# Kernel tuning notes

Measured on AMD Instinct MI355X. Metric: run time of the kernel, lower is better.

## Reference

```python
import jax, jax.numpy as jnp
import numpy as np

B, P, G = 64, 512, 64      # batch of independent nets, populations, generator inputs
N = P + G                   # presynaptic channels per population
H = 32                      # neuron-MLP hidden width
DT = 0.1                    # integration step (ms)
EREV_MIN, EREV_MAX = -75.0, 0.0


def setup_inputs() -> dict:
    key = jax.random.key(0)
    ks = jax.random.split(key, 16)
    state = jax.random.uniform(ks[0], (B, P), dtype=jnp.float32)          # prev firing rates
    inp = jax.random.uniform(ks[1], (B, G), dtype=jnp.float32)            # generator rates
    R = jnp.ones((B, P, N), dtype=jnp.float32)                            # recovered resources
    U = jnp.zeros((B, P, N), dtype=jnp.float32)                           # utilization
    A = jnp.zeros((B, P, N), dtype=jnp.float32)                           # active resources
    gsyn_max = 2.0 * jax.random.uniform(ks[2], (P, N), dtype=jnp.float32)
    pconn = jax.random.uniform(ks[3], (P, N), dtype=jnp.float32)
    Uinc = 0.1 + 0.5 * jax.random.uniform(ks[4], (P, N), dtype=jnp.float32)
    tau_r = 100.0 + 400.0 * jax.random.uniform(ks[5], (P, N), dtype=jnp.float32)  # recovery (ms)
    tau_f = 10.0 + 50.0 * jax.random.uniform(ks[6], (P, N), dtype=jnp.float32)    # facilitation
    tau_d = 2.0 + 5.0 * jax.random.uniform(ks[7], (P, N), dtype=jnp.float32)      # decay
    Erev = jnp.where(jax.random.uniform(ks[8], (P, N)) > 0.5, 0.0, -75.0).astype(jnp.float32)
    mask = jnp.ones((P, N), dtype=bool)                                   # is_connected_mask
    Cm = 0.5 + 2.0 * jax.random.uniform(ks[9], (P,), dtype=jnp.float32)
    W1 = 0.5 * jax.random.normal(ks[10], (P, 2, H), dtype=jnp.float32)
    b1 = 0.5 * jax.random.normal(ks[11], (P, H), dtype=jnp.float32)
    W2 = 0.5 * jax.random.normal(ks[12], (P, H, 1), dtype=jnp.float32)
    b2 = 0.5 * jax.random.normal(ks[13], (P, 1), dtype=jnp.float32)
    return {"state": state, "inp": inp, "R": R, "U": U, "A": A,
            "gsyn_max": gsyn_max, "pconn": pconn, "Uinc": Uinc,
            "tau_r": tau_r, "tau_f": tau_f, "tau_d": tau_d,
            "Erev": Erev, "mask": mask, "Cm": Cm,
            "W1": W1, "b1": b1, "W2": W2, "b2": b2}


def reference(state, inp, R, U, A, gsyn_max, pconn, Uinc, tau_r, tau_f, tau_d,
              Erev, mask, Cm, W1, b1, W2, b2):
    # --- TimeStepLayer.call: concat prev state with generator input -> full presyn vector
    x = jnp.concatenate([state, inp], axis=-1)                  # [B, N]
    SR = x[:, None, :] * pconn                                  # [B, P, N] spike prob per conn

    # --- TsodycsMarkramSynapse one Euler step (all populations fused)
    e_d = jnp.exp(-DT / tau_d)
    e_r = jnp.exp(-DT / tau_r)
    e_f = jnp.exp(-DT / tau_f)
    tau1r = jnp.where(tau_d != tau_r, tau_d / (tau_d - tau_r), 1e-13)
    a_dec = A * e_d
    r_dec = 1.0 + (R - 1.0 + tau1r * U) * e_r - tau1r * U
    u_dec = U * e_f
    u0 = u_dec + Uinc * (1.0 - u_dec) * SR                      # new utilization
    a0 = a_dec + u0 * r_dec * SR                                # new active fraction

    # --- synaptic drive features per population
    g = gsyn_max * a0 * mask                                    # [B, P, N]
    g_tot = jnp.sum(g, axis=-1)                                 # [B, P]
    E_eff = jnp.sum(g * Erev, axis=-1) / (g_tot + 1e-8)
    E_norm = (E_eff - EREV_MIN) / (EREV_MAX - EREV_MIN)
    g_norm = g_tot / (g_tot + Cm[None, :])
    feat = jnp.stack([E_norm, g_norm], axis=-1)                 # [B, P, 2]

    # --- frozen per-population neuron net (square activation, sigmoid rate)
    h = jnp.square(jnp.einsum('bpf,pfh->bph', feat, W1) + b1)   # [B, P, H]
    out = jax.nn.sigmoid(jnp.einsum('bph,pho->bpo', h, W2) + b2)[..., 0]  # [B, P]
    return out
```

## Files before the change

kernel.cpp:

```cpp
#include <hip/hip_runtime.h>

#define PP 512
#define GG 64
#define NN 576

#define STEP(PC, UP, EF, ER, C1, ED, GS, GEp, Rv, Uv, Av, Xv, GT, GE)        \
  {                                                                          \
    float sr   = (Xv) * (PC);                                                \
    float udec = (Uv) * (EF);                                                \
    float u0   = udec + (UP) * (Xv) * (1.0f - udec);                         \
    float rdec = 1.0f + ((Rv) - 1.0f) * (ER) + (C1) * (Uv);                  \
    float a0   = (Av) * (ED) + u0 * rdec * sr;                               \
    GT = fmaf((GS), a0, GT);                                                 \
    GE = fmaf((GEp), a0, GE);                                                \
  }

__global__ __launch_bounds__(256, 4)
void timestep_kernel(const float* __restrict__ state,
                     const float* __restrict__ inp,
                     const float* __restrict__ R,
                     const float* __restrict__ U,
                     const float* __restrict__ A,
                     const float* __restrict__ gsyn_max,
                     const float* __restrict__ pconn,
                     const float* __restrict__ Uinc,
                     const float* __restrict__ tau_r,
                     const float* __restrict__ tau_f,
                     const float* __restrict__ tau_d,
                     const float* __restrict__ Erev,
                     const float* __restrict__ Cm,
                     const float* __restrict__ W1,
                     const float* __restrict__ b1,
                     const float* __restrict__ W2,
                     const float* __restrict__ b2,
                     float* __restrict__ out)
{
    __shared__ __align__(16) float Ppc[NN];
    __shared__ __align__(16) float Pup[NN];
    __shared__ __align__(16) float Pef[NN];
    __shared__ __align__(16) float Per[NN];
    __shared__ __align__(16) float Pc1[NN];
    __shared__ __align__(16) float Ped[NN];
    __shared__ __align__(16) float Pgs[NN];
    __shared__ __align__(16) float PgE[NN];

    const int tid  = threadIdx.x;
    const int lane = tid & 63;
    const int wave = tid >> 6;
    const int p    = blockIdx.x >> 1;
    const int half = blockIdx.x & 1;
    const int prow = p * NN;

    #pragma unroll
    for (int k = 0; k < 3; ++k) {
        int n = tid + k * 256;
        if (k < 2 || tid < 64) {
            const int o = prow + n;
            float tr = tau_r[o], tf = tau_f[o], td = tau_d[o];
            float pcv = pconn[o], ui = Uinc[o], gsv = gsyn_max[o], erv = Erev[o];
            float e_r = __expf(-0.1f * __builtin_amdgcn_rcpf(tr));
            float e_f = __expf(-0.1f * __builtin_amdgcn_rcpf(tf));
            float e_d = __expf(-0.1f * __builtin_amdgcn_rcpf(td));
            float diff = td - tr;
            float t1r  = (diff != 0.0f) ? td * __builtin_amdgcn_rcpf(diff) : 1e-13f;
            Ppc[n] = pcv;
            Pup[n] = ui * pcv;
            Pef[n] = e_f;
            Per[n] = e_r;
            Pc1[n] = t1r * (e_r - 1.0f);
            Ped[n] = e_d;
            Pgs[n] = gsv;
            PgE[n] = gsv * erv;
        }
    }

    const int   j   = lane & 31;
    const float w1a = W1[p * 64 + j];
    const float w1b = W1[p * 64 + 32 + j];
    const float b1j = b1[p * 32 + j];
    const float w2j = W2[p * 32 + j];
    const float b2p = b2[p];
    const float cmp = Cm[p];

    __syncthreads();

    const int bbase = half * 32 + wave * 8;
    #pragma unroll 1
    for (int pass = 0; pass < 4; ++pass) {
        const int b0  = bbase + pass * 2;
        const int b1i = b0 + 1;
        const size_t r0 = ((size_t)b0  * PP + p) * (size_t)NN;
        const size_t r1 = ((size_t)b1i * PP + p) * (size_t)NN;
        float gt0 = 0.0f, ge0 = 0.0f, gt1 = 0.0f, ge1 = 0.0f;

        #pragma unroll
        for (int c = 0; c < 2; ++c) {
            const int off = c * 64 + lane;
            const int np  = c * 256 + 4 * lane;
            float4 Ra = ((const float4*)R)[(r0 >> 2) + off];
            float4 Rb = ((const float4*)R)[(r1 >> 2) + off];
            float4 Ua = ((const float4*)U)[(r0 >> 2) + off];
            float4 Ub = ((const float4*)U)[(r1 >> 2) + off];
            float4 Aa = ((const float4*)A)[(r0 >> 2) + off];
            float4 Ab = ((const float4*)A)[(r1 >> 2) + off];
            float4 Xa = ((const float4*)state)[((b0  * PP) >> 2) + off];
            float4 Xb = ((const float4*)state)[((b1i * PP) >> 2) + off];
            float4 vpc = *(const float4*)&Ppc[np];
            float4 vup = *(const float4*)&Pup[np];
            float4 vef = *(const float4*)&Pef[np];
            float4 ver = *(const float4*)&Per[np];
            float4 vc1 = *(const float4*)&Pc1[np];
            float4 ved = *(const float4*)&Ped[np];
            float4 vgs = *(const float4*)&Pgs[np];
            float4 vgE = *(const float4*)&PgE[np];
            STEP(vpc.x, vup.x, vef.x, ver.x, vc1.x, ved.x, vgs.x, vgE.x,
                 Ra.x, Ua.x, Aa.x, Xa.x, gt0, ge0)
            STEP(vpc.y, vup.y, vef.y, ver.y, vc1.y, ved.y, vgs.y, vgE.y,
                 Ra.y, Ua.y, Aa.y, Xa.y, gt0, ge0)
            STEP(vpc.z, vup.z, vef.z, ver.z, vc1.z, ved.z, vgs.z, vgE.z,
                 Ra.z, Ua.z, Aa.z, Xa.z, gt0, ge0)
            STEP(vpc.w, vup.w, vef.w, ver.w, vc1.w, ved.w, vgs.w, vgE.w,
                 Ra.w, Ua.w, Aa.w, Xa.w, gt0, ge0)
            STEP(vpc.x, vup.x, vef.x, ver.x, vc1.x, ved.x, vgs.x, vgE.x,
                 Rb.x, Ub.x, Ab.x, Xb.x, gt1, ge1)
            STEP(vpc.y, vup.y, vef.y, ver.y, vc1.y, ved.y, vgs.y, vgE.y,
                 Rb.y, Ub.y, Ab.y, Xb.y, gt1, ge1)
            STEP(vpc.z, vup.z, vef.z, ver.z, vc1.z, ved.z, vgs.z, vgE.z,
                 Rb.z, Ub.z, Ab.z, Xb.z, gt1, ge1)
            STEP(vpc.w, vup.w, vef.w, ver.w, vc1.w, ved.w, vgs.w, vgE.w,
                 Rb.w, Ub.w, Ab.w, Xb.w, gt1, ge1)
        }
        {
            const int    nt = 512 + lane;
            const size_t oa = r0 + (size_t)nt;
            const size_t ob = r1 + (size_t)nt;
            float Rs0 = R[oa], Us0 = U[oa], As0 = A[oa];
            float Rs1 = R[ob], Us1 = U[ob], As1 = A[ob];
            float Xs0 = inp[b0  * GG + lane];
            float Xs1 = inp[b1i * GG + lane];
            float spc = Ppc[nt], sup = Pup[nt], sef = Pef[nt], ser = Per[nt];
            float sc1 = Pc1[nt], sed = Ped[nt], sgs = Pgs[nt], sgE = PgE[nt];
            STEP(spc, sup, sef, ser, sc1, sed, sgs, sgE,
                 Rs0, Us0, As0, Xs0, gt0, ge0)
            STEP(spc, sup, sef, ser, sc1, sed, sgs, sgE,
                 Rs1, Us1, As1, Xs1, gt1, ge1)
        }

        #pragma unroll
        for (int m = 32; m >= 1; m >>= 1) {
            gt0 += __shfl_xor(gt0, m, 64);
            gt1 += __shfl_xor(gt1, m, 64);
            ge0 += __shfl_xor(ge0, m, 64);
            ge1 += __shfl_xor(ge1, m, 64);
        }

        float En0 = (ge0 * __builtin_amdgcn_rcpf(gt0 + 1e-8f) + 75.0f) * (1.0f / 75.0f);
        float En1 = (ge1 * __builtin_amdgcn_rcpf(gt1 + 1e-8f) + 75.0f) * (1.0f / 75.0f);
        float gn0 = gt0 * __builtin_amdgcn_rcpf(gt0 + cmp);
        float gn1 = gt1 * __builtin_amdgcn_rcpf(gt1 + cmp);
        float pre0 = fmaf(En0, w1a, fmaf(gn0, w1b, b1j));
        float pre1 = fmaf(En1, w1a, fmaf(gn1, w1b, b1j));
        float v0 = pre0 * pre0 * w2j;
        float v1 = pre1 * pre1 * w2j;
        #pragma unroll
        for (int m = 16; m >= 1; m >>= 1) {
            v0 += __shfl_xor(v0, m, 64);
            v1 += __shfl_xor(v1, m, 64);
        }
        float s0 = v0 + b2p;
        float s1 = v1 + b2p;
        float o0 = __builtin_amdgcn_rcpf(1.0f + __expf(-s0));
        float o1 = __builtin_amdgcn_rcpf(1.0f + __expf(-s1));
        if (lane == 0) {
            out[(size_t)b0  * PP + p] = o0;
            out[(size_t)b1i * PP + p] = o1;
        }
    }
}

extern "C" void kernel_launch(void* const* d_in, const int* in_sizes, int n_in,
                              void* d_out, int out_size, void* d_ws, size_t ws_size,
                              hipStream_t stream) {
    const float* state = (const float*)d_in[0];
    const float* inp   = (const float*)d_in[1];
    const float* R     = (const float*)d_in[2];
    const float* U     = (const float*)d_in[3];
    const float* A     = (const float*)d_in[4];
    const float* gsyn  = (const float*)d_in[5];
    const float* pconn = (const float*)d_in[6];
    const float* Uinc  = (const float*)d_in[7];
    const float* taur  = (const float*)d_in[8];
    const float* tauf  = (const float*)d_in[9];
    const float* taud  = (const float*)d_in[10];
    const float* Erev  = (const float*)d_in[11];
    const float* Cm    = (const float*)d_in[13];
    const float* W1    = (const float*)d_in[14];
    const float* b1    = (const float*)d_in[15];
    const float* W2    = (const float*)d_in[16];
    const float* b2    = (const float*)d_in[17];
    float* out = (float*)d_out;

    hipLaunchKernelGGL(timestep_kernel, dim3(1024), dim3(256), 0, stream,
                       state, inp, R, U, A, gsyn, pconn, Uinc, taur, tauf, taud,
                       Erev, Cm, W1, b1, W2, b2, out);
}
```

Measured before the change: 282.5 us.

## Split batch across four blocks per population and fully unroll four batches per wave

Each population is now handled by four blocks of 16 batches instead of two blocks of 32, doubling the grid to 2048 blocks. Each wave processes four batch rows in one straight-line body, with all loads issued up front, replacing the rolled loop of two-row passes. The intent is more parallelism and more memory loads in flight to saturate HBM bandwidth on the streaming R/U/A reads. The cost is that the per-population parameter precompute (exp and reciprocal) is done twice as often, plus more register pressure now that the occupancy hint is gone from launch bounds.

```diff
diff --git a/kernel.cpp b/kernel.cpp
--- a/kernel.cpp
+++ b/kernel.cpp
@@ -15,7 +15,70 @@
     GE = fmaf((GEp), a0, GE);                                                \
   }
 
-__global__ __launch_bounds__(256, 4)
+#define PASSBODY(bb, GT, GE)                                                 \
+  {                                                                          \
+    const int b_  = (bb);                                                    \
+    const int r4_ = (b_ * PP + p) * (NN / 4);                                \
+    const int s4_ = (b_ * PP) >> 2;                                          \
+    float4 Ra = ((const float4*)R)[r4_ + lane];                              \
+    float4 Ua = ((const float4*)U)[r4_ + lane];                              \
+    float4 Aa = ((const float4*)A)[r4_ + lane];                              \
+    float4 Xa = ((const float4*)state)[s4_ + lane];                          \
+    float4 Rb = ((const float4*)R)[r4_ + 64 + lane];                         \
+    float4 Ub = ((const float4*)U)[r4_ + 64 + lane];                         \
+    float4 Ab = ((const float4*)A)[r4_ + 64 + lane];                         \
+    float4 Xb = ((const float4*)state)[s4_ + 64 + lane];                     \
+    const int ot_ = r4_ * 4 + 512 + lane;                                    \
+    float Rs = R[ot_];                                                       \
+    float Us = U[ot_];                                                       \
+    float As = A[ot_];                                                       \
+    float Xs = inp[b_ * GG + lane];                                          \
+    {                                                                        \
+      const int np = 4 * lane;                                               \
+      float4 vpc = *(const float4*)&Ppc[np];                                 \
+      float4 vup = *(const float4*)&Pup[np];                                 \
+      float4 vef = *(const float4*)&Pef[np];                                 \
+      float4 ver = *(const float4*)&Per[np];                                 \
+      float4 vc1 = *(const float4*)&Pc1[np];                                 \
+      float4 ved = *(const float4*)&Ped[np];                                 \
+      float4 vgs = *(const float4*)&Pgs[np];                                 \
+      float4 vgE = *(const float4*)&PgE[np];                                 \
+      STEP(vpc.x, vup.x, vef.x, ver.x, vc1.x, ved.x, vgs.x, vgE.x,           \
+           Ra.x, Ua.x, Aa.x, Xa.x, GT, GE)                                   \
+      STEP(vpc.y, vup.y, vef.y, ver.y, vc1.y, ved.y, vgs.y, vgE.y,           \
+           Ra.y, Ua.y, Aa.y, Xa.y, GT, GE)                                   \
+      STEP(vpc.z, vup.z, vef.z, ver.z, vc1.z, ved.z, vgs.z, vgE.z,           \
+           Ra.z, Ua.z, Aa.z, Xa.z, GT, GE)                                   \
+      STEP(vpc.w, vup.w, vef.w, ver.w, vc1.w, ved.w, vgs.w, vgE.w,           \
+           Ra.w, Ua.w, Aa.w, Xa.w, GT, GE)                                   \
+    }                                                                        \
+    {                                                                        \
+      const int np = 256 + 4 * lane;                                         \
+      float4 vpc = *(const float4*)&Ppc[np];                                 \
+      float4 vup = *(const float4*)&Pup[np];                                 \
+      float4 vef = *(const float4*)&Pef[np];                                 \
+      float4 ver = *(const float4*)&Per[np];                                 \
+      float4 vc1 = *(const float4*)&Pc1[np];                                 \
+      float4 ved = *(const float4*)&Ped[np];                                 \
+      float4 vgs = *(const float4*)&Pgs[np];                                 \
+      float4 vgE = *(const float4*)&PgE[np];                                 \
+      STEP(vpc.x, vup.x, vef.x, ver.x, vc1.x, ved.x, vgs.x, vgE.x,           \
+           Rb.x, Ub.x, Ab.x, Xb.x, GT, GE)                                   \
+      STEP(vpc.y, vup.y, vef.y, ver.y, vc1.y, ved.y, vgs.y, vgE.y,           \
+           Rb.y, Ub.y, Ab.y, Xb.y, GT, GE)                                   \
+      STEP(vpc.z, vup.z, vef.z, ver.z, vc1.z, ved.z, vgs.z, vgE.z,           \
+           Rb.z, Ub.z, Ab.z, Xb.z, GT, GE)                                   \
+      STEP(vpc.w, vup.w, vef.w, ver.w, vc1.w, ved.w, vgs.w, vgE.w,           \
+           Rb.w, Ub.w, Ab.w, Xb.w, GT, GE)                                   \
+    }                                                                        \
+    {                                                                        \
+      const int nt = 512 + lane;                                             \
+      STEP(Ppc[nt], Pup[nt], Pef[nt], Per[nt], Pc1[nt], Ped[nt],             \
+           Pgs[nt], PgE[nt], Rs, Us, As, Xs, GT, GE)                         \
+    }                                                                        \
+  }
+
+__global__ __launch_bounds__(256)
 void timestep_kernel(const float* __restrict__ state,
                      const float* __restrict__ inp,
                      const float* __restrict__ R,
@@ -47,8 +110,8 @@
     const int tid  = threadIdx.x;
     const int lane = tid & 63;
     const int wave = tid >> 6;
-    const int p    = blockIdx.x >> 1;
-    const int half = blockIdx.x & 1;
+    const int p    = blockIdx.x >> 2;
+    const int q    = blockIdx.x & 3;
     const int prow = p * NN;
 
     #pragma unroll
@@ -84,97 +147,57 @@
 
     __syncthreads();
 
-    const int bbase = half * 32 + wave * 8;
-    #pragma unroll 1
-    for (int pass = 0; pass < 4; ++pass) {
-        const int b0  = bbase + pass * 2;
-        const int b1i = b0 + 1;
-        const size_t r0 = ((size_t)b0  * PP + p) * (size_t)NN;
-        const size_t r1 = ((size_t)b1i * PP + p) * (size_t)NN;
-        float gt0 = 0.0f, ge0 = 0.0f, gt1 = 0.0f, ge1 = 0.0f;
-
-        #pragma unroll
-        for (int c = 0; c < 2; ++c) {
-            const int off = c * 64 + lane;
-            const int np  = c * 256 + 4 * lane;
-            float4 Ra = ((const float4*)R)[(r0 >> 2) + off];
-            float4 Rb = ((const float4*)R)[(r1 >> 2) + off];
-            float4 Ua = ((const float4*)U)[(r0 >> 2) + off];
-            float4 Ub = ((const float4*)U)[(r1 >> 2) + off];
-            float4 Aa = ((const float4*)A)[(r0 >> 2) + off];
-            float4 Ab = ((const float4*)A)[(r1 >> 2) + off];
-            float4 Xa = ((const float4*)state)[((b0  * PP) >> 2) + off];
-            float4 Xb = ((const float4*)state)[((b1i * PP) >> 2) + off];
-            float4 vpc = *(const float4*)&Ppc[np];
-            float4 vup = *(const float4*)&Pup[np];
-            float4 vef = *(const float4*)&Pef[np];
-            float4 ver = *(const float4*)&Per[np];
-            float4 vc1 = *(const float4*)&Pc1[np];
-            float4 ved = *(const float4*)&Ped[np];
-            float4 vgs = *(const float4*)&Pgs[np];
-            float4 vgE = *(const float4*)&PgE[np];
-            STEP(vpc.x, vup.x, vef.x, ver.x, vc1.x, ved.x, vgs.x, vgE.x,
-                 Ra.x, Ua.x, Aa.x, Xa.x, gt0, ge0)
-            STEP(vpc.y, vup.y, vef.y, ver.y, vc1.y, ved.y, vgs.y, vgE.y,
-                 Ra.y, Ua.y, Aa.y, Xa.y, gt0, ge0)
-            STEP(vpc.z, vup.z, vef.z, ver.z, vc1.z, ved.z, vgs.z, vgE.z,
-                 Ra.z, Ua.z, Aa.z, Xa.z, gt0, ge0)
-            STEP(vpc.w, vup.w, vef.w, ver.w, vc1.w, ved.w, vgs.w, vgE.w,
-                 Ra.w, Ua.w, Aa.w, Xa.w, gt0, ge0)
-            STEP(vpc.x, vup.x, vef.x, ver.x, vc1.x, ved.x, vgs.x, vgE.x,
-                 Rb.x, Ub.x, Ab.x, Xb.x, gt1, ge1)
-            STEP(vpc.y, vup.y, vef.y, ver.y, vc1.y, ved.y, vgs.y, vgE.y,
-                 Rb.y, Ub.y, Ab.y, Xb.y, gt1, ge1)
-            STEP(vpc.z, vup.z, vef.z, ver.z, vc1.z, ved.z, vgs.z, vgE.z,
-                 Rb.z, Ub.z, Ab.z, Xb.z, gt1, ge1)
-            STEP(vpc.w, vup.w, vef.w, ver.w, vc1.w, ved.w, vgs.w, vgE.w,
-                 Rb.w, Ub.w, Ab.w, Xb.w, gt1, ge1)
-        }
-        {
-            const int    nt = 512 + lane;
-            const size_t oa = r0 + (size_t)nt;
-            const size_t ob = r1 + (size_t)nt;
-            float Rs0 = R[oa], Us0 = U[oa], As0 = A[oa];
-            float Rs1 = R[ob], Us1 = U[ob], As1 = A[ob];
-            float Xs0 = inp[b0  * GG + lane];
-            float Xs1 = inp[b1i * GG + lane];
-            float spc = Ppc[nt], sup = Pup[nt], sef = Pef[nt], ser = Per[nt];
-            float sc1 = Pc1[nt], sed = Ped[nt], sgs = Pgs[nt], sgE = PgE[nt];
-            STEP(spc, sup, sef, ser, sc1, sed, sgs, sgE,
-                 Rs0, Us0, As0, Xs0, gt0, ge0)
-            STEP(spc, sup, sef, ser, sc1, sed, sgs, sgE,
-                 Rs1, Us1, As1, Xs1, gt1, ge1)
-        }
-
-        #pragma unroll
-        for (int m = 32; m >= 1; m >>= 1) {
-            gt0 += __shfl_xor(gt0, m, 64);
-            gt1 += __shfl_xor(gt1, m, 64);
-            ge0 += __shfl_xor(ge0, m, 64);
-            ge1 += __shfl_xor(ge1, m, 64);
-        }
-
-        float En0 = (ge0 * __builtin_amdgcn_rcpf(gt0 + 1e-8f) + 75.0f) * (1.0f / 75.0f);
-        float En1 = (ge1 * __builtin_amdgcn_rcpf(gt1 + 1e-8f) + 75.0f) * (1.0f / 75.0f);
-        float gn0 = gt0 * __builtin_amdgcn_rcpf(gt0 + cmp);
-        float gn1 = gt1 * __builtin_amdgcn_rcpf(gt1 + cmp);
-        float pre0 = fmaf(En0, w1a, fmaf(gn0, w1b, b1j));
-        float pre1 = fmaf(En1, w1a, fmaf(gn1, w1b, b1j));
-        float v0 = pre0 * pre0 * w2j;
-        float v1 = pre1 * pre1 * w2j;
-        #pragma unroll
-        for (int m = 16; m >= 1; m >>= 1) {
-            v0 += __shfl_xor(v0, m, 64);
-            v1 += __shfl_xor(v1, m, 64);
-        }
-        float s0 = v0 + b2p;
-        float s1 = v1 + b2p;
-        float o0 = __builtin_amdgcn_rcpf(1.0f + __expf(-s0));
-        float o1 = __builtin_amdgcn_rcpf(1.0f + __expf(-s1));
-        if (lane == 0) {
-            out[(size_t)b0  * PP + p] = o0;
-            out[(size_t)b1i * PP + p] = o1;
-        }
+    const int bbase = q * 16 + wave * 4;
+    float gt0 = 0.0f, ge0 = 0.0f;
+    float gt1 = 0.0f, ge1 = 0.0f;
+    float gt2 = 0.0f, ge2 = 0.0f;
+    float gt3 = 0.0f, ge3 = 0.0f;
+    PASSBODY(bbase + 0, gt0, ge0)
+    PASSBODY(bbase + 1, gt1, ge1)
+    PASSBODY(bbase + 2, gt2, ge2)
+    PASSBODY(bbase + 3, gt3, ge3)
+
+    #pragma unroll
+    for (int m = 32; m >= 1; m >>= 1) {
+        gt0 += __shfl_xor(gt0, m, 64);
+        gt1 += __shfl_xor(gt1, m, 64);
+        gt2 += __shfl_xor(gt2, m, 64);
+        gt3 += __shfl_xor(gt3, m, 64);
+        ge0 += __shfl_xor(ge0, m, 64);
+        ge1 += __shfl_xor(ge1, m, 64);
+        ge2 += __shfl_xor(ge2, m, 64);
+        ge3 += __shfl_xor(ge3, m, 64);
+    }
+
+    float En0 = (ge0 * __builtin_amdgcn_rcpf(gt0 + 1e-8f) + 75.0f) * (1.0f / 75.0f);
+    float En1 = (ge1 * __builtin_amdgcn_rcpf(gt1 + 1e-8f) + 75.0f) * (1.0f / 75.0f);
+    float En2 = (ge2 * __builtin_amdgcn_rcpf(gt2 + 1e-8f) + 75.0f) * (1.0f / 75.0f);
+    float En3 = (ge3 * __builtin_amdgcn_rcpf(gt3 + 1e-8f) + 75.0f) * (1.0f / 75.0f);
+    float gn0 = gt0 * __builtin_amdgcn_rcpf(gt0 + cmp);
+    float gn1 = gt1 * __builtin_amdgcn_rcpf(gt1 + cmp);
+    float gn2 = gt2 * __builtin_amdgcn_rcpf(gt2 + cmp);
+    float gn3 = gt3 * __builtin_amdgcn_rcpf(gt3 + cmp);
+    float pre0 = fmaf(En0, w1a, fmaf(gn0, w1b, b1j));
+    float pre1 = fmaf(En1, w1a, fmaf(gn1, w1b, b1j));
+    float pre2 = fmaf(En2, w1a, fmaf(gn2, w1b, b1j));
+    float pre3 = fmaf(En3, w1a, fmaf(gn3, w1b, b1j));
+    float v0 = pre0 * pre0 * w2j;
+    float v1 = pre1 * pre1 * w2j;
+    float v2 = pre2 * pre2 * w2j;
+    float v3 = pre3 * pre3 * w2j;
+    #pragma unroll
+    for (int m = 16; m >= 1; m >>= 1) {
+        v0 += __shfl_xor(v0, m, 64);
+        v1 += __shfl_xor(v1, m, 64);
+        v2 += __shfl_xor(v2, m, 64);
+        v3 += __shfl_xor(v3, m, 64);
+    }
+    if (lane == 0) {
+        const int ob = bbase * PP + p;
+        out[ob]          = __builtin_amdgcn_rcpf(1.0f + __expf(-(v0 + b2p)));
+        out[ob + PP]     = __builtin_amdgcn_rcpf(1.0f + __expf(-(v1 + b2p)));
+        out[ob + 2 * PP] = __builtin_amdgcn_rcpf(1.0f + __expf(-(v2 + b2p)));
+        out[ob + 3 * PP] = __builtin_amdgcn_rcpf(1.0f + __expf(-(v3 + b2p)));
     }
 }
 
@@ -200,7 +223,7 @@
     const float* b2    = (const float*)d_in[17];
     float* out = (float*)d_out;
 
-    hipLaunchKernelGGL(timestep_kernel, dim3(1024), dim3(256), 0, stream,
+    hipLaunchKernelGGL(timestep_kernel, dim3(2048), dim3(256), 0, stream,
                        state, inp, R, U, A, gsyn, pconn, Uinc, taur, tauf, taud,
                        Erev, Cm, W1, b1, W2, b2, out);
 }
```

Result: faster. 256.0 us (-9.4%).
